# Kernel optimization log

Hardware: AMD Instinct MI355X
Metric: run time of the kernel (lower is better)

The kernel has to match this reference:

```python
import jax, jax.numpy as jnp
import numpy as np
from jax import lax

NUM_LAYERS = 16
NUM_NEIGHBORS = 4
NUM_CHANNELS = 8
RESIDUAL_SCALE = 1.0


def _build_kernel(w, num_neighbors):
    # w: (C, Nn+1) -> (C, 1, K, K) cross-stencil depthwise kernel
    C = w.shape[0]
    Nn = num_neighbors
    K = 2 * Nn + 1
    mid = Nn
    k = jnp.zeros((C, K, K), dtype=w.dtype)
    k = k.at[:, mid, mid].set(w[:, 0])
    for d in range(1, Nn + 1):
        v = w[:, d]
        k = k.at[:, mid, mid + d].set(v)
        k = k.at[:, mid, mid - d].set(v)
        k = k.at[:, mid + d, mid].set(v)
        k = k.at[:, mid - d, mid].set(v)
    return k[:, None, :, :]


def _apply_layer(x, w, num_neighbors):
    # x: (B, C, L, L) circular depthwise conv with cross-stencil kernel
    C = x.shape[1]
    kernel = _build_kernel(w, num_neighbors)
    p = num_neighbors
    x_pad = jnp.pad(x, ((0, 0), (0, 0), (p, p), (p, p)), mode='wrap')
    return lax.conv_general_dilated(
        x_pad, kernel, window_strides=(1, 1), padding='VALID',
        feature_group_count=C, dimension_numbers=('NCHW', 'OIHW', 'NCHW'))


def _celu(x):
    # alpha = 1.0
    return jnp.maximum(x, 0.0) + jnp.expm1(jnp.minimum(x, 0.0))


def setup_inputs() -> dict:
    key = jax.random.key(0)
    k_n, k_w = jax.random.split(key)
    n = jax.random.normal(k_n, (256, 128, 3), dtype=jnp.float32)
    # godslayer laplacian init for weights (num_layers, C, Nn+1)
    shape = (NUM_LAYERS, NUM_CHANNELS, NUM_NEIGHBORS + 1)
    depth = jnp.sqrt(float(NUM_LAYERS))
    neigh = jnp.sqrt(float(max(1, NUM_NEIGHBORS)))
    w = jnp.zeros(shape, dtype=jnp.float32)
    w = w.at[:, :, 0].set(-0.15 / depth)
    w = w.at[:, :, 1:].set(0.04 / (depth * neigh))
    w = w + 0.01 * jax.random.normal(k_w, shape, dtype=jnp.float32)
    return {"n": n, "weights": w}


def reference(n, weights):
    # gram matrix: (B, L, L), zero diagonal
    B, L, _ = n.shape
    g = jnp.einsum('bia,bja->bij', n, n)
    g = g * (1.0 - jnp.eye(L, dtype=g.dtype))
    # broadcast over channels -> (B, C, L, L)
    x0 = jnp.broadcast_to(g[:, None, :, :], (B, NUM_CHANNELS, L, L))
    s = jnp.asarray(RESIDUAL_SCALE, dtype=x0.dtype)

    def layer_forward(x_in, w):
        y = _apply_layer(x_in, w, NUM_NEIGHBORS)
        return x_in + s * _celu(y), None

    x_final, _ = lax.scan(layer_forward, x0, weights)
    out = jnp.mean(x_final, axis=(-1, -2, -3))  # (B,)
    return jnp.exp(-out)
```

## Files before the change

kernel.cpp:

```cpp
#include <hip/hip_runtime.h>
#include <math.h>

#define LSZ 128
#define NCH 8
#define NLAY 16
#define LOG2E 1.4426950408889634f
#define LN2   0.6931471805599453f

typedef float f4 __attribute__((ext_vector_type(4)));
typedef float f2 __attribute__((ext_vector_type(2)));

__device__ __forceinline__ float uni(float v) {
    return __uint_as_float(__builtin_amdgcn_readfirstlane(__float_as_uint(v)));
}

__global__ __launch_bounds__(1024)
void plane_kernel(const float* __restrict__ nrm,
                  const float* __restrict__ W,
                  float* __restrict__ ws)
{
    __shared__ float xa[LSZ * LSZ];
    __shared__ float xb[LSZ * LSZ];
    __shared__ float nsm[LSZ * 3];
    __shared__ float wsm[NLAY * 5];
    __shared__ float red[16];

    const int bid = blockIdx.x;
    const int b   = bid >> 3;
    const int c   = bid & 7;
    const int tid = threadIdx.x;

    if (tid < LSZ * 3) nsm[tid] = nrm[b * (LSZ * 3) + tid];
    if (tid < NLAY * 5) {
        int l = tid / 5, d = tid % 5;
        wsm[tid] = W[l * (NCH * 5) + c * 5 + d] * LOG2E;
    }
    __syncthreads();

    const int jg = tid & 31;
    const int is = tid >> 5;
    const int j0 = jg * 4;
    const int i0 = is * 4;

    f4 own[4];

    {
        float nj0x = nsm[(j0 + 0) * 3 + 0], nj0y = nsm[(j0 + 0) * 3 + 1], nj0z = nsm[(j0 + 0) * 3 + 2];
        float nj1x = nsm[(j0 + 1) * 3 + 0], nj1y = nsm[(j0 + 1) * 3 + 1], nj1z = nsm[(j0 + 1) * 3 + 2];
        float nj2x = nsm[(j0 + 2) * 3 + 0], nj2y = nsm[(j0 + 2) * 3 + 1], nj2z = nsm[(j0 + 2) * 3 + 2];
        float nj3x = nsm[(j0 + 3) * 3 + 0], nj3y = nsm[(j0 + 3) * 3 + 1], nj3z = nsm[(j0 + 3) * 3 + 2];
#pragma unroll
        for (int k = 0; k < 4; ++k) {
            int r = i0 + k;
            float n0 = nsm[r * 3 + 0], n1 = nsm[r * 3 + 1], n2 = nsm[r * 3 + 2];
            float g0 = n0 * nj0x + n1 * nj0y + n2 * nj0z;
            float g1 = n0 * nj1x + n1 * nj1y + n2 * nj1z;
            float g2 = n0 * nj2x + n1 * nj2y + n2 * nj2z;
            float g3 = n0 * nj3x + n1 * nj3y + n2 * nj3z;
            if (r == j0 + 0) g0 = 0.f;
            if (r == j0 + 1) g1 = 0.f;
            if (r == j0 + 2) g2 = 0.f;
            if (r == j0 + 3) g3 = 0.f;
            f4 v = (f4){g0, g1, g2, g3};
            *(f4*)&xa[r * LSZ + j0] = v;
            own[k] = v;
        }
    }
    __syncthreads();

    const int oT = ((i0 - 4) & (LSZ - 1)) * LSZ + j0;
    const int oB = ((i0 + 4) & (LSZ - 1)) * LSZ + j0;
    const int oL = i0 * LSZ + ((j0 - 4) & (LSZ - 1));
    const int oR = i0 * LSZ + ((j0 + 4) & (LSZ - 1));
    const int oO = i0 * LSZ + j0;

    auto do_layer = [&](const float* src, float* dst, int l) {
        const float w0 = uni(wsm[l * 5 + 0]);
        const float w1 = uni(wsm[l * 5 + 1]);
        const float w2 = uni(wsm[l * 5 + 2]);
        const float w3 = uni(wsm[l * 5 + 3]);
        const float w4 = uni(wsm[l * 5 + 4]);
        const float sT = -(float)l * (w0 + 4.0f * (w1 + w2 + w3 + w4));

        f4 t[4], bo[4], res[4];
#pragma unroll
        for (int k = 0; k < 4; ++k) {
            t[k]  = *(const f4*)&src[oT + k * LSZ];
            bo[k] = *(const f4*)&src[oB + k * LSZ];
        }

#define VV(k) ((k) < 4 ? t[(k)] : (k) < 8 ? own[(k) - 4] : bo[(k) - 8])

        f4 Lc = *(const f4*)&src[oL];
        f4 Rc = *(const f4*)&src[oR];
#pragma unroll
        for (int m = 0; m < 4; ++m) {
            f4 Ln, Rn;
            if (m < 3) {
                Ln = *(const f4*)&src[oL + (m + 1) * LSZ];
                Rn = *(const f4*)&src[oR + (m + 1) * LSZ];
            }
            const f4 C = own[m];

            f2 h1m = C.xy + C.zw;
            f4 h1 = (f4){Lc.w + C.y, h1m.x, h1m.y, C.z + Rc.x};
            f2 h2a = Lc.zw + C.zw;
            f2 h2b = C.xy + Rc.xy;
            f4 h2 = (f4){h2a.x, h2a.y, h2b.x, h2b.y};
            f2 h3m = Lc.zw + Rc.xy;
            f4 h3 = (f4){Lc.y + C.w, h3m.x, h3m.y, C.x + Rc.z};
            f4 h4 = Lc + Rc;

            f4 y = (w0 * C + sT)
                 + w1 * (h1 + (VV(m + 3) + VV(m + 5)))
                 + w2 * (h2 + (VV(m + 2) + VV(m + 6)))
                 + w3 * (h3 + (VV(m + 1) + VV(m + 7)))
                 + w4 * (h4 + (VV(m + 0) + VV(m + 8)));

            f4 yp = __builtin_elementwise_max(y, (f4)0.0f);
            f4 yn = __builtin_elementwise_min(y, (f4)0.0f);
            f4 e2;
            e2.x = __builtin_amdgcn_exp2f(yn.x);
            e2.y = __builtin_amdgcn_exp2f(yn.y);
            e2.z = __builtin_amdgcn_exp2f(yn.z);
            e2.w = __builtin_amdgcn_exp2f(yn.w);
            f4 r = (yp * LN2 + C) + e2;

            *(f4*)&dst[oO + m * LSZ] = r;
            res[m] = r;

            Lc = Ln; Rc = Rn;
        }
#undef VV
#pragma unroll
        for (int m = 0; m < 4; ++m) own[m] = res[m];
        __syncthreads();
    };

#pragma unroll 1
    for (int l = 0; l < NLAY; l += 2) {
        do_layer(xa, xb, l);
        do_layer(xb, xa, l + 1);
    }

    float local = 0.f;
#pragma unroll
    for (int m = 0; m < 4; ++m)
        local += own[m].x + own[m].y + own[m].z + own[m].w;

#pragma unroll
    for (int off = 32; off > 0; off >>= 1)
        local += __shfl_down(local, off, 64);

    const int wave = tid >> 6;
    if ((tid & 63) == 0) red[wave] = local;
    __syncthreads();
    if (tid == 0) {
        float s = 0.f;
#pragma unroll
        for (int w = 0; w < 16; ++w) s += red[w];
        ws[bid] = s;
    }
}

__global__ void finish_kernel(const float* __restrict__ ws, float* __restrict__ out) {
    int b = threadIdx.x;
    float s = 0.f;
#pragma unroll
    for (int c = 0; c < NCH; ++c) s += ws[b * NCH + c];
    out[b] = expf(16.0f - s / (8.0f * 128.0f * 128.0f));
}

extern "C" void kernel_launch(void* const* d_in, const int* in_sizes, int n_in,
                              void* d_out, int out_size, void* d_ws, size_t ws_size,
                              hipStream_t stream) {
    const float* nrm = (const float*)d_in[0];
    const float* W   = (const float*)d_in[1];
    float* out = (float*)d_out;
    float* ws  = (float*)d_ws;

    plane_kernel<<<dim3(256 * NCH), dim3(1024), 0, stream>>>(nrm, W, ws);
    finish_kernel<<<dim3(1), dim3(256), 0, stream>>>(ws, out);
}
```

Before: 274.4 us.

## Store stencil planes as bf16 in LDS and halve threads with 4x8 tiles

```diff
diff --git a/kernel.cpp b/kernel.cpp
--- a/kernel.cpp
+++ b/kernel.cpp
@@ -14,16 +14,45 @@
     return __uint_as_float(__builtin_amdgcn_readfirstlane(__float_as_uint(v)));
 }
 
-__global__ __launch_bounds__(1024)
+__device__ __forceinline__ f2 unpk2(unsigned u) {
+    f2 r;
+    r.x = __uint_as_float(u << 16);
+    r.y = __uint_as_float(u & 0xffff0000u);
+    return r;
+}
+struct f8 { f4 a, b; };
+__device__ __forceinline__ f8 ldr8(const unsigned short* p) {
+    uint4 w = *(const uint4*)p;
+    f2 p0 = unpk2(w.x), p1 = unpk2(w.y), p2 = unpk2(w.z), p3 = unpk2(w.w);
+    f8 r;
+    r.a = (f4){p0.x, p0.y, p1.x, p1.y};
+    r.b = (f4){p2.x, p2.y, p3.x, p3.y};
+    return r;
+}
+__device__ __forceinline__ f4 ldr4(const unsigned short* p) {
+    uint2 w = *(const uint2*)p;
+    f2 p0 = unpk2(w.x), p1 = unpk2(w.y);
+    return (f4){p0.x, p0.y, p1.x, p1.y};
+}
+__device__ __forceinline__ void str8(unsigned short* p, f4 va, f4 vb) {
+    unsigned q0, q1, q2, q3;
+    asm("v_cvt_pk_bf16_f32 %0, %1, %2" : "=v"(q0) : "v"(va.x), "v"(va.y));
+    asm("v_cvt_pk_bf16_f32 %0, %1, %2" : "=v"(q1) : "v"(va.z), "v"(va.w));
+    asm("v_cvt_pk_bf16_f32 %0, %1, %2" : "=v"(q2) : "v"(vb.x), "v"(vb.y));
+    asm("v_cvt_pk_bf16_f32 %0, %1, %2" : "=v"(q3) : "v"(vb.z), "v"(vb.w));
+    *(uint4*)p = make_uint4(q0, q1, q2, q3);
+}
+
+__global__ __launch_bounds__(512)
 void plane_kernel(const float* __restrict__ nrm,
                   const float* __restrict__ W,
                   float* __restrict__ ws)
 {
-    __shared__ float xa[LSZ * LSZ];
-    __shared__ float xb[LSZ * LSZ];
+    __shared__ __align__(16) unsigned short xa[LSZ * LSZ];
+    __shared__ __align__(16) unsigned short xb[LSZ * LSZ];
     __shared__ float nsm[LSZ * 3];
     __shared__ float wsm[NLAY * 5];
-    __shared__ float red[16];
+    __shared__ float red[8];
 
     const int bid = blockIdx.x;
     const int b   = bid >> 3;
@@ -37,33 +66,31 @@
     }
     __syncthreads();
 
-    const int jg = tid & 31;
-    const int is = tid >> 5;
-    const int j0 = jg * 4;
+    const int jg = tid & 15;
+    const int is = tid >> 4;
+    const int j0 = jg * 8;
     const int i0 = is * 4;
 
-    f4 own[4];
-
     {
-        float nj0x = nsm[(j0 + 0) * 3 + 0], nj0y = nsm[(j0 + 0) * 3 + 1], nj0z = nsm[(j0 + 0) * 3 + 2];
-        float nj1x = nsm[(j0 + 1) * 3 + 0], nj1y = nsm[(j0 + 1) * 3 + 1], nj1z = nsm[(j0 + 1) * 3 + 2];
-        float nj2x = nsm[(j0 + 2) * 3 + 0], nj2y = nsm[(j0 + 2) * 3 + 1], nj2z = nsm[(j0 + 2) * 3 + 2];
-        float nj3x = nsm[(j0 + 3) * 3 + 0], nj3y = nsm[(j0 + 3) * 3 + 1], nj3z = nsm[(j0 + 3) * 3 + 2];
+        float njx[8], njy[8], njz[8];
+#pragma unroll
+        for (int q = 0; q < 8; ++q) {
+            njx[q] = nsm[(j0 + q) * 3 + 0];
+            njy[q] = nsm[(j0 + q) * 3 + 1];
+            njz[q] = nsm[(j0 + q) * 3 + 2];
+        }
 #pragma unroll
         for (int k = 0; k < 4; ++k) {
             int r = i0 + k;
             float n0 = nsm[r * 3 + 0], n1 = nsm[r * 3 + 1], n2 = nsm[r * 3 + 2];
-            float g0 = n0 * nj0x + n1 * nj0y + n2 * nj0z;
-            float g1 = n0 * nj1x + n1 * nj1y + n2 * nj1z;
-            float g2 = n0 * nj2x + n1 * nj2y + n2 * nj2z;
-            float g3 = n0 * nj3x + n1 * nj3y + n2 * nj3z;
-            if (r == j0 + 0) g0 = 0.f;
-            if (r == j0 + 1) g1 = 0.f;
-            if (r == j0 + 2) g2 = 0.f;
-            if (r == j0 + 3) g3 = 0.f;
-            f4 v = (f4){g0, g1, g2, g3};
-            *(f4*)&xa[r * LSZ + j0] = v;
-            own[k] = v;
+            float g[8];
+#pragma unroll
+            for (int q = 0; q < 8; ++q) {
+                g[q] = n0 * njx[q] + n1 * njy[q] + n2 * njz[q];
+                if (r == j0 + q) g[q] = 0.f;
+            }
+            str8(&xa[r * LSZ + j0], (f4){g[0], g[1], g[2], g[3]},
+                                    (f4){g[4], g[5], g[6], g[7]});
         }
     }
     __syncthreads();
@@ -71,10 +98,12 @@
     const int oT = ((i0 - 4) & (LSZ - 1)) * LSZ + j0;
     const int oB = ((i0 + 4) & (LSZ - 1)) * LSZ + j0;
     const int oL = i0 * LSZ + ((j0 - 4) & (LSZ - 1));
-    const int oR = i0 * LSZ + ((j0 + 4) & (LSZ - 1));
+    const int oR = i0 * LSZ + ((j0 + 8) & (LSZ - 1));
     const int oO = i0 * LSZ + j0;
 
-    auto do_layer = [&](const float* src, float* dst, int l) {
+    float lsum = 0.f;
+
+    auto do_layer = [&](const unsigned short* src, unsigned short* dst, int l) {
         const float w0 = uni(wsm[l * 5 + 0]);
         const float w1 = uni(wsm[l * 5 + 1]);
         const float w2 = uni(wsm[l * 5 + 2]);
@@ -82,58 +111,68 @@
         const float w4 = uni(wsm[l * 5 + 4]);
         const float sT = -(float)l * (w0 + 4.0f * (w1 + w2 + w3 + w4));
 
-        f4 t[4], bo[4], res[4];
+        f4 ta[4], tb[4], oa[4], ob[4], ba[4], bb[4];
 #pragma unroll
         for (int k = 0; k < 4; ++k) {
-            t[k]  = *(const f4*)&src[oT + k * LSZ];
-            bo[k] = *(const f4*)&src[oB + k * LSZ];
-        }
-
-#define VV(k) ((k) < 4 ? t[(k)] : (k) < 8 ? own[(k) - 4] : bo[(k) - 8])
-
-        f4 Lc = *(const f4*)&src[oL];
-        f4 Rc = *(const f4*)&src[oR];
+            f8 r;
+            r = ldr8(&src[oT + k * LSZ]); ta[k] = r.a; tb[k] = r.b;
+            r = ldr8(&src[oO + k * LSZ]); oa[k] = r.a; ob[k] = r.b;
+            r = ldr8(&src[oB + k * LSZ]); ba[k] = r.a; bb[k] = r.b;
+        }
+
+#define VA(k) ((k) < 4 ? ta[(k)] : (k) < 8 ? oa[(k) - 4] : ba[(k) - 8])
+#define VB(k) ((k) < 4 ? tb[(k)] : (k) < 8 ? ob[(k) - 4] : bb[(k) - 8])
+
 #pragma unroll
         for (int m = 0; m < 4; ++m) {
-            f4 Ln, Rn;
-            if (m < 3) {
-                Ln = *(const f4*)&src[oL + (m + 1) * LSZ];
-                Rn = *(const f4*)&src[oR + (m + 1) * LSZ];
+            const f4 A = ldr4(&src[oL + m * LSZ]);
+            const f4 D = ldr4(&src[oR + m * LSZ]);
+            const f4 B = oa[m], C = ob[m];
+
+            f4 h1a; { f2 t = B.xy + B.zw; h1a = (f4){A.w + B.y, t.x, t.y, B.z + C.x}; }
+            f4 h2a; { f2 u = A.zw + B.zw; f2 v = B.xy + C.xy; h2a = (f4){u.x, u.y, v.x, v.y}; }
+            f4 h3a; { f2 t = A.zw + C.xy; h3a = (f4){A.y + B.w, t.x, t.y, B.x + C.z}; }
+            f4 h4a = A + C;
+            f4 h1b; { f2 t = C.xy + C.zw; h1b = (f4){B.w + C.y, t.x, t.y, C.z + D.x}; }
+            f4 h2b; { f2 u = B.zw + C.zw; f2 v = C.xy + D.xy; h2b = (f4){u.x, u.y, v.x, v.y}; }
+            f4 h3b; { f2 t = B.zw + D.xy; h3b = (f4){B.y + C.w, t.x, t.y, C.x + D.z}; }
+            f4 h4b = B + D;
+
+            f4 ya = (w0 * B + sT)
+                  + w1 * (h1a + (VA(m + 3) + VA(m + 5)))
+                  + w2 * (h2a + (VA(m + 2) + VA(m + 6)))
+                  + w3 * (h3a + (VA(m + 1) + VA(m + 7)))
+                  + w4 * (h4a + (VA(m + 0) + VA(m + 8)));
+            f4 yb = (w0 * C + sT)
+                  + w1 * (h1b + (VB(m + 3) + VB(m + 5)))
+                  + w2 * (h2b + (VB(m + 2) + VB(m + 6)))
+                  + w3 * (h3b + (VB(m + 1) + VB(m + 7)))
+                  + w4 * (h4b + (VB(m + 0) + VB(m + 8)));
+
+            f4 ypa = __builtin_elementwise_max(ya, (f4)0.0f);
+            f4 yna = __builtin_elementwise_min(ya, (f4)0.0f);
+            f4 ypb = __builtin_elementwise_max(yb, (f4)0.0f);
+            f4 ynb = __builtin_elementwise_min(yb, (f4)0.0f);
+            f4 ea, eb;
+            ea.x = __builtin_amdgcn_exp2f(yna.x);
+            ea.y = __builtin_amdgcn_exp2f(yna.y);
+            ea.z = __builtin_amdgcn_exp2f(yna.z);
+            ea.w = __builtin_amdgcn_exp2f(yna.w);
+            eb.x = __builtin_amdgcn_exp2f(ynb.x);
+            eb.y = __builtin_amdgcn_exp2f(ynb.y);
+            eb.z = __builtin_amdgcn_exp2f(ynb.z);
+            eb.w = __builtin_amdgcn_exp2f(ynb.w);
+            f4 ra = (ypa * LN2 + B) + ea;
+            f4 rb = (ypb * LN2 + C) + eb;
+
+            str8(&dst[oO + m * LSZ], ra, rb);
+            if (l == NLAY - 1) {
+                f4 s = ra + rb;
+                lsum += (s.x + s.y) + (s.z + s.w);
             }
-            const f4 C = own[m];
-
-            f2 h1m = C.xy + C.zw;
-            f4 h1 = (f4){Lc.w + C.y, h1m.x, h1m.y, C.z + Rc.x};
-            f2 h2a = Lc.zw + C.zw;
-            f2 h2b = C.xy + Rc.xy;
-            f4 h2 = (f4){h2a.x, h2a.y, h2b.x, h2b.y};
-            f2 h3m = Lc.zw + Rc.xy;
-            f4 h3 = (f4){Lc.y + C.w, h3m.x, h3m.y, C.x + Rc.z};
-            f4 h4 = Lc + Rc;
-
-            f4 y = (w0 * C + sT)
-                 + w1 * (h1 + (VV(m + 3) + VV(m + 5)))
-                 + w2 * (h2 + (VV(m + 2) + VV(m + 6)))
-                 + w3 * (h3 + (VV(m + 1) + VV(m + 7)))
-                 + w4 * (h4 + (VV(m + 0) + VV(m + 8)));
-
-            f4 yp = __builtin_elementwise_max(y, (f4)0.0f);
-            f4 yn = __builtin_elementwise_min(y, (f4)0.0f);
-            f4 e2;
-            e2.x = __builtin_amdgcn_exp2f(yn.x);
-            e2.y = __builtin_amdgcn_exp2f(yn.y);
-            e2.z = __builtin_amdgcn_exp2f(yn.z);
-            e2.w = __builtin_amdgcn_exp2f(yn.w);
-            f4 r = (yp * LN2 + C) + e2;
-
-            *(f4*)&dst[oO + m * LSZ] = r;
-            res[m] = r;
-
-            Lc = Ln; Rc = Rn;
-        }
-#undef VV
-#pragma unroll
-        for (int m = 0; m < 4; ++m) own[m] = res[m];
+        }
+#undef VA
+#undef VB
         __syncthreads();
     };
 
@@ -143,11 +182,7 @@
         do_layer(xb, xa, l + 1);
     }
 
-    float local = 0.f;
-#pragma unroll
-    for (int m = 0; m < 4; ++m)
-        local += own[m].x + own[m].y + own[m].z + own[m].w;
-
+    float local = lsum;
 #pragma unroll
     for (int off = 32; off > 0; off >>= 1)
         local += __shfl_down(local, off, 64);
@@ -158,7 +193,7 @@
     if (tid == 0) {
         float s = 0.f;
 #pragma unroll
-        for (int w = 0; w < 16; ++w) s += red[w];
+        for (int w = 0; w < 8; ++w) s += red[w];
         ws[bid] = s;
     }
 }
@@ -179,6 +214,6 @@
     float* out = (float*)d_out;
     float* ws  = (float*)d_ws;
 
-    plane_kernel<<<dim3(256 * NCH), dim3(1024), 0, stream>>>(nrm, W, ws);
+    plane_kernel<<<dim3(256 * NCH), dim3(512), 0, stream>>>(nrm, W, ws);
     finish_kernel<<<dim3(1), dim3(256), 0, stream>>>(ws, out);
 }
```

New measurement: 355.5 us. 1.3x slower.
